# Optimization experiments

Hardware: AMD Instinct MI355X
Metric: run time of the kernel (lower is better)

## Reference

```python
import jax, jax.numpy as jnp
import numpy as np

NU = 160000   # users
NM = 60000    # movies
D = 64        # embedding dim
E = 5000000   # rating edges
L = 200000    # label edges to score
NUM_LAYERS = 3


def setup_inputs() -> dict:
    key = jax.random.key(0)
    k1, k2, k3, k4, k5, k6 = jax.random.split(key, 6)
    return {
        "emb_user": jax.random.normal(k1, (NU, D), jnp.float32),
        "emb_movie": jax.random.normal(k2, (NM, D), jnp.float32),
        "node_id_user": jnp.arange(NU),
        "node_id_movie": jnp.arange(NM),
        "edge_from": jax.random.randint(k3, (E,), 0, NM),   # movie side of each edge
        "edge_to": jax.random.randint(k4, (E,), 0, NU),     # user side of each edge
        "label_movie": jax.random.randint(k5, (L,), 0, NM),
        "label_user": jax.random.randint(k6, (L,), 0, NU),
    }


def reference(emb_user, emb_movie, node_id_user, node_id_movie,
              edge_from, edge_to, label_movie, label_user):
    # Embedding lookup (node_id is an arange over all nodes in the batch)
    x_u = emb_user[node_id_user]    # [NU, D]
    x_m = emb_movie[node_id_movie]  # [NM, D]

    # Symmetric degree normalization: deg(from)^-1/2 * deg(to)^-1/2 per edge
    ones = jnp.ones(edge_from.shape[0], dtype=x_m.dtype)
    deg_m = jax.ops.segment_sum(ones, edge_from, num_segments=NM)
    deg_u = jax.ops.segment_sum(ones, edge_to, num_segments=NU)
    inv_m = jnp.where(deg_m > 0, deg_m ** -0.5, 0.0)
    inv_u = jnp.where(deg_u > 0, deg_u ** -0.5, 0.0)
    norm = inv_m[edge_from] * inv_u[edge_to]  # [E]

    # NOTE: the original torch code never writes the propagated embeddings back
    # into x_dict, so every layer propagates the layer-0 embeddings. Replicated
    # faithfully here.
    embs_u = [x_u]
    embs_m = [x_m]
    for _ in range(NUM_LAYERS):
        # movie -> user aggregation (x2y): gather movie feats, scale, scatter-add to users
        u_agg = jax.ops.segment_sum(norm[:, None] * x_m[edge_from], edge_to, num_segments=NU)
        m_agg = jax.ops.segment_sum(norm[:, None] * x_u[edge_to], edge_from, num_segments=NM)
        embs_u.append(u_agg)
        embs_m.append(m_agg)

    # Layer combination with weights 1/(l+1)
    w = 1.0 / (jnp.arange(NUM_LAYERS + 1, dtype=x_u.dtype) + 1.0)
    res_u = jnp.einsum('l,lnd->nd', w, jnp.stack(embs_u))  # [NU, D]
    res_m = jnp.einsum('l,lnd->nd', w, jnp.stack(embs_m))  # [NM, D]

    # Classifier: dot product over label edges
    scores = jnp.sum(res_u[label_user] * res_m[label_movie], axis=-1)  # [L]
    return (scores, res_u, res_m)
```

## Files before the change

### kernel.cpp

```cpp
#include <hip/hip_runtime.h>

#define NU 160000
#define NM 60000
#define DD 64
#define NE 5000000
#define NL 200000

#define COEF (13.0f / 12.0f)

#define SHIFT_U 9
#define SHIFT_M 7
#define NBU ((NU + (1 << SHIFT_U) - 1) >> SHIFT_U)
#define NBM ((NM + (1 << SHIFT_M) - 1) >> SHIFT_M)


#define CEC 16

__global__ void bucket_count_kernel(const int* __restrict__ ef, const int* __restrict__ et,
                                    int* __restrict__ gbh_u, int* __restrict__ gbh_m) {
    __shared__ int bhu[NBU], bhm[NBM];
    int tid = threadIdx.x;
    for (int i = tid; i < NBU; i += 256) bhu[i] = 0;
    for (int i = tid; i < NBM; i += 256) bhm[i] = 0;
    __syncthreads();
    int base = (blockIdx.x * 256 + tid) * CEC;
    if (base < NE) {
        const int4* f4 = (const int4*)(ef + base);
        const int4* t4 = (const int4*)(et + base);
        #pragma unroll
        for (int q = 0; q < CEC / 4; q++) {
            int4 ff = f4[q]; int4 tt = t4[q];
            atomicAdd(&bhm[ff.x >> SHIFT_M], 1); atomicAdd(&bhu[tt.x >> SHIFT_U], 1);
            atomicAdd(&bhm[ff.y >> SHIFT_M], 1); atomicAdd(&bhu[tt.y >> SHIFT_U], 1);
            atomicAdd(&bhm[ff.z >> SHIFT_M], 1); atomicAdd(&bhu[tt.z >> SHIFT_U], 1);
            atomicAdd(&bhm[ff.w >> SHIFT_M], 1); atomicAdd(&bhu[tt.w >> SHIFT_U], 1);
        }
    }
    __syncthreads();
    for (int i = tid; i < NBU; i += 256) if (bhu[i]) atomicAdd(&gbh_u[i], bhu[i]);
    for (int i = tid; i < NBM; i += 256) if (bhm[i]) atomicAdd(&gbh_m[i], bhm[i]);
}


__global__ void scan_small_kernel(const int* __restrict__ in, int* __restrict__ out,
                                  int* __restrict__ cur, int n) {
    __shared__ int buf[256];
    int tid = threadIdx.x;
    int idx = tid * 4;
    int v0 = (idx + 0 < n) ? in[idx + 0] : 0;
    int v1 = (idx + 1 < n) ? in[idx + 1] : 0;
    int v2 = (idx + 2 < n) ? in[idx + 2] : 0;
    int v3 = (idx + 3 < n) ? in[idx + 3] : 0;
    int s = v0 + v1 + v2 + v3;
    buf[tid] = s;
    __syncthreads();
    for (int off = 1; off < 256; off <<= 1) {
        int t = (tid >= off) ? buf[tid - off] : 0;
        __syncthreads();
        buf[tid] += t;
        __syncthreads();
    }
    int p = buf[tid] - s;
    if (idx + 0 < n) { out[idx + 0] = p; if (cur) cur[idx + 0] = p; p += v0; }
    if (idx + 1 < n) { out[idx + 1] = p; if (cur) cur[idx + 1] = p; p += v1; }
    if (idx + 2 < n) { out[idx + 2] = p; if (cur) cur[idx + 2] = p; p += v2; }
    if (idx + 3 < n) { out[idx + 3] = p; if (cur) cur[idx + 3] = p; p += v3; }
    if (tid == 255) out[n] = buf[255];
}


#define PEC 16

__global__ void partition_kernel(const int* __restrict__ key, const int* __restrict__ val,
                                 int* __restrict__ bcur, int2* __restrict__ stage,
                                 int shift, int nb) {
    __shared__ int lh[512];
    __shared__ int lbase[512];
    int tid = threadIdx.x;
    for (int i = tid; i < nb; i += 256) lh[i] = 0;
    __syncthreads();
    int base = (blockIdx.x * 256 + tid) * PEC;
    int k_[PEC], v_[PEC], br_[PEC];
    bool act = base < NE;
    if (act) {
        const int4* k4 = (const int4*)(key + base);
        const int4* v4 = (const int4*)(val + base);
        #pragma unroll
        for (int q = 0; q < PEC / 4; q++) {
            int4 kk = k4[q]; int4 vv = v4[q];
            k_[q * 4 + 0] = kk.x; k_[q * 4 + 1] = kk.y; k_[q * 4 + 2] = kk.z; k_[q * 4 + 3] = kk.w;
            v_[q * 4 + 0] = vv.x; v_[q * 4 + 1] = vv.y; v_[q * 4 + 2] = vv.z; v_[q * 4 + 3] = vv.w;
        }
        #pragma unroll
        for (int q = 0; q < PEC; q++) {
            int b = k_[q] >> shift;
            int r = atomicAdd(&lh[b], 1);
            br_[q] = (b << 13) | r;
        }
    }
    __syncthreads();
    for (int i = tid; i < nb; i += 256) lbase[i] = lh[i] ? atomicAdd(&bcur[i], lh[i]) : 0;
    __syncthreads();
    if (act) {
        #pragma unroll
        for (int q = 0; q < PEC; q++) {
            int b = br_[q] >> 13;
            int r = br_[q] & 8191;
            stage[lbase[b] + r] = make_int2(k_[q], v_[q]);
        }
    }
}


__global__ void build_kernel(const int2* __restrict__ stage, const int* __restrict__ bo,
                             float* __restrict__ inv, int* __restrict__ rp,
                             int* __restrict__ pay, int shift, int n) {
    __shared__ int cnt[512];
    __shared__ int tmp[512];
    int b = blockIdx.x;
    int tid = threadIdx.x;
    int bs = 1 << shift;
    int base = b << shift;
    int nn = min(bs, n - base);
    int s0 = bo[b];
    int s1 = bo[b + 1];

    for (int i = tid; i < bs; i += 256) cnt[i] = 0;
    __syncthreads();
    for (int e = s0 + tid; e < s1; e += 256)
        atomicAdd(&cnt[stage[e].x - base], 1);
    __syncthreads();
    int o0 = (tid < bs) ? cnt[tid] : 0;
    int o1 = (tid + 256 < bs) ? cnt[tid + 256] : 0;
    for (int off = 1; off < bs; off <<= 1) {
        for (int i = tid; i < bs; i += 256) tmp[i] = (i >= off) ? cnt[i - off] : 0;
        __syncthreads();
        for (int i = tid; i < bs; i += 256) cnt[i] += tmp[i];
        __syncthreads();
    }
    if (tid < bs) {
        int excl = cnt[tid] - o0;
        tmp[tid] = s0 + excl;
        if (tid < nn) {
            rp[base + tid] = s0 + excl;
            inv[base + tid] = (o0 > 0) ? rsqrtf((float)o0) : 0.0f;
        }
    }
    if (tid + 256 < bs) {
        int i = tid + 256;
        int excl = cnt[i] - o1;
        tmp[i] = s0 + excl;
        if (i < nn) {
            rp[base + i] = s0 + excl;
            inv[base + i] = (o1 > 0) ? rsqrtf((float)o1) : 0.0f;
        }
    }
    if (b == 0 && tid == 0) rp[n] = NE;
    __syncthreads();
    for (int e = s0 + tid; e < s1; e += 256) {
        int2 p = stage[e];
        int pos = atomicAdd(&tmp[p.x - base], 1);
        pay[pos] = p.y;
    }
}


__global__ void gather_kernel(const int* __restrict__ rp, const int* __restrict__ pay,
                              const float* __restrict__ inv_dst, const float* __restrict__ inv_src,
                              const float* __restrict__ x_src, const float* __restrict__ x_dst,
                              float* __restrict__ res, int n) {
    int tid = blockIdx.x * blockDim.x + threadIdx.x;
    int node = tid >> 6;
    int lane = threadIdx.x & 63;
    if (node >= n) return;
    int start = rp[node];
    int end   = rp[node + 1];
    float acc = 0.0f;
    for (int i = start; i < end; i += 64) {
        int cnt = min(end - i, 64);
        int nid = (lane < cnt) ? pay[i + lane] : 0;
        int j = 0;
        for (; j + 4 <= cnt; j += 4) {
            int f0 = __shfl(nid, j + 0, 64);
            int f1 = __shfl(nid, j + 1, 64);
            int f2 = __shfl(nid, j + 2, 64);
            int f3 = __shfl(nid, j + 3, 64);
            float w0 = inv_src[f0], w1 = inv_src[f1], w2 = inv_src[f2], w3 = inv_src[f3];
            float a0 = x_src[f0 * DD + lane];
            float a1 = x_src[f1 * DD + lane];
            float a2 = x_src[f2 * DD + lane];
            float a3 = x_src[f3 * DD + lane];
            acc += w0 * a0 + w1 * a1 + w2 * a2 + w3 * a3;
        }
        for (; j < cnt; j++) {
            int f0 = __shfl(nid, j, 64);
            acc += inv_src[f0] * x_src[f0 * DD + lane];
        }
    }
    int o = node * DD + lane;
    res[o] = x_dst[o] + COEF * inv_dst[node] * acc;
}


__global__ void score_kernel(const int* __restrict__ lm, const int* __restrict__ lu,
                             const float* __restrict__ ru, const float* __restrict__ rm,
                             float* __restrict__ scores) {
    int tid = blockIdx.x * blockDim.x + threadIdx.x;
    int l = tid >> 6;
    int d = threadIdx.x & 63;
    if (l < NL) {
        int u = lu[l];
        int m = lm[l];
        float v = ru[u * DD + d] * rm[m * DD + d];
        #pragma unroll
        for (int off = 32; off >= 1; off >>= 1)
            v += __shfl_down(v, off, 64);
        if (d == 0) scores[l] = v;
    }
}


__global__ void degree_kernel_f(const int* __restrict__ ef, const int* __restrict__ et,
                                float* __restrict__ deg_m, float* __restrict__ deg_u) {
    int i = blockIdx.x * blockDim.x + threadIdx.x;
    if (i < NE) {
        atomicAdd(&deg_m[ef[i]], 1.0f);
        atomicAdd(&deg_u[et[i]], 1.0f);
    }
}

__global__ void inv_kernel_f(float* __restrict__ deg, int n) {
    int i = blockIdx.x * blockDim.x + threadIdx.x;
    if (i < n) {
        float d = deg[i];
        deg[i] = (d > 0.0f) ? (1.0f / sqrtf(d)) : 0.0f;
    }
}

__global__ void agg_kernel_f(const int* __restrict__ ef, const int* __restrict__ et,
                             const float* __restrict__ inv_m, const float* __restrict__ inv_u,
                             const float* __restrict__ x_u, const float* __restrict__ x_m,
                             float* __restrict__ res_u, float* __restrict__ res_m) {
    int tid = blockIdx.x * blockDim.x + threadIdx.x;
    int e = tid >> 6;
    int d = tid & 63;
    if (e < NE) {
        int f = ef[e];
        int t = et[e];
        float norm = inv_m[f] * inv_u[t] * COEF;
        atomicAdd(&res_u[t * DD + d], norm * x_m[f * DD + d]);
        atomicAdd(&res_m[f * DD + d], norm * x_u[t * DD + d]);
    }
}

__global__ void add_base_kernel_f(const float* __restrict__ xu, const float* __restrict__ xm,
                                  float* __restrict__ ru, float* __restrict__ rm) {
    int i = blockIdx.x * blockDim.x + threadIdx.x;
    const int nu = NU * DD;
    const int nm = NM * DD;
    if (i < nu) {
        ru[i] += xu[i];
    } else if (i < nu + nm) {
        int j = i - nu;
        rm[j] += xm[j];
    }
}


extern "C" void kernel_launch(void* const* d_in, const int* in_sizes, int n_in,
                              void* d_out, int out_size, void* d_ws, size_t ws_size,
                              hipStream_t stream) {
    const float* emb_user  = (const float*)d_in[0];
    const float* emb_movie = (const float*)d_in[1];
    const int* edge_from   = (const int*)d_in[4];
    const int* edge_to     = (const int*)d_in[5];
    const int* label_movie = (const int*)d_in[6];
    const int* label_user  = (const int*)d_in[7];

    float* out    = (float*)d_out;
    float* scores = out;
    float* res_u  = out + NL;
    float* res_m  = out + NL + (size_t)NU * DD;

    int*   gbh_u  = (int*)d_ws;
    int*   gbh_m  = gbh_u + NBU;
    int*   bo_u   = gbh_m + NBM;
    int*   bcur_u = bo_u + NBU + 1;
    int*   bo_m   = bcur_u + NBU;
    int*   bcur_m = bo_m + NBM + 1;
    float* inv_u  = (float*)(bcur_m + NBM);
    float* inv_m  = inv_u + NU;
    int*   rp_u   = (int*)(inv_m + NM);
    int*   rp_m   = rp_u + NU + 1;
    int*   pay_u  = rp_m + NM + 1;
    int*   pay_m  = pay_u + NE;
    size_t off    = (size_t)((pay_m + NE) - (int*)d_ws);
    off = (off + 3) & ~(size_t)3;
    int2*  stage  = (int2*)((int*)d_ws + off);

    size_t needed = (off + 2 * (size_t)NE) * sizeof(int);

    if (ws_size >= needed) {
        hipMemsetAsync(gbh_u, 0, (size_t)(NBU + NBM) * sizeof(int), stream);

        bucket_count_kernel<<<(NE / CEC + 255) / 256, 256, 0, stream>>>(
            edge_from, edge_to, gbh_u, gbh_m);
        scan_small_kernel<<<1, 256, 0, stream>>>(gbh_u, bo_u, bcur_u, NBU);
        scan_small_kernel<<<1, 256, 0, stream>>>(gbh_m, bo_m, bcur_m, NBM);

        partition_kernel<<<(NE / PEC + 255) / 256, 256, 0, stream>>>(
            edge_to, edge_from, bcur_u, stage, SHIFT_U, NBU);
        build_kernel<<<NBU, 256, 0, stream>>>(stage, bo_u, inv_u, rp_u, pay_u, SHIFT_U, NU);

        partition_kernel<<<(NE / PEC + 255) / 256, 256, 0, stream>>>(
            edge_from, edge_to, bcur_m, stage, SHIFT_M, NBM);
        build_kernel<<<NBM, 256, 0, stream>>>(stage, bo_m, inv_m, rp_m, pay_m, SHIFT_M, NM);

        gather_kernel<<<((size_t)NU * 64 + 255) / 256, 256, 0, stream>>>(
            rp_u, pay_u, inv_u, inv_m, emb_movie, emb_user, res_u, NU);
        gather_kernel<<<((size_t)NM * 64 + 255) / 256, 256, 0, stream>>>(
            rp_m, pay_m, inv_m, inv_u, emb_user, emb_movie, res_m, NM);
    } else {
        float* fdeg_u = (float*)d_ws;
        float* fdeg_m = fdeg_u + NU;
        hipMemsetAsync(res_u, 0, (size_t)(NU + NM) * DD * sizeof(float), stream);
        hipMemsetAsync(fdeg_u, 0, (size_t)(NU + NM) * sizeof(float), stream);
        degree_kernel_f<<<(NE + 255) / 256, 256, 0, stream>>>(edge_from, edge_to, fdeg_m, fdeg_u);
        inv_kernel_f<<<(NU + NM + 255) / 256, 256, 0, stream>>>(fdeg_u, NU + NM);
        agg_kernel_f<<<((size_t)NE * 64 + 255) / 256, 256, 0, stream>>>(
            edge_from, edge_to, fdeg_m, fdeg_u, emb_user, emb_movie, res_u, res_m);
        add_base_kernel_f<<<((NU + NM) * DD + 255) / 256, 256, 0, stream>>>(
            emb_user, emb_movie, res_u, res_m);
    }

    score_kernel<<<((size_t)NL * 64 + 255) / 256, 256, 0, stream>>>(
        label_movie, label_user, res_u, res_m, scores);
}
```

Measured before the change: 749.5 us.

## Pack staging edges into one int and gather bf16 pre-scaled source features

Edge staging now packs the local destination index and the source id into a single 32-bit word instead of an int2, which halves staging traffic in partition and build. A new prescale kernel multiplies each source embedding by its inverse-sqrt degree and stores the result as bf16. The gather then reads half-width rows with no per-edge weight lookup. This cuts the random-gather bandwidth, at the cost of bf16 rounding error in the aggregated embeddings and an extra prescale pass that reuses the staging buffer region.

```diff
diff --git a/kernel.cpp b/kernel.cpp
--- a/kernel.cpp
+++ b/kernel.cpp
@@ -1,4 +1,5 @@
 #include <hip/hip_runtime.h>
+#include <hip/hip_bf16.h>
 
 #define NU 160000
 #define NM 60000
@@ -12,6 +13,8 @@
 #define SHIFT_M 7
 #define NBU ((NU + (1 << SHIFT_U) - 1) >> SHIFT_U)
 #define NBM ((NM + (1 << SHIFT_M) - 1) >> SHIFT_M)
+#define VB_U 16
+#define VB_M 18
 
 
 #define CEC 16
@@ -72,11 +75,12 @@
 #define PEC 16
 
 __global__ void partition_kernel(const int* __restrict__ key, const int* __restrict__ val,
-                                 int* __restrict__ bcur, int2* __restrict__ stage,
-                                 int shift, int nb) {
+                                 int* __restrict__ bcur, int* __restrict__ stage,
+                                 int shift, int nb, int valbits) {
     __shared__ int lh[512];
     __shared__ int lbase[512];
     int tid = threadIdx.x;
+    int lmask = (1 << shift) - 1;
     for (int i = tid; i < nb; i += 256) lh[i] = 0;
     __syncthreads();
     int base = (blockIdx.x * 256 + tid) * PEC;
@@ -106,15 +110,15 @@
         for (int q = 0; q < PEC; q++) {
             int b = br_[q] >> 13;
             int r = br_[q] & 8191;
-            stage[lbase[b] + r] = make_int2(k_[q], v_[q]);
-        }
-    }
-}
-
-
-__global__ void build_kernel(const int2* __restrict__ stage, const int* __restrict__ bo,
+            stage[lbase[b] + r] = ((k_[q] & lmask) << valbits) | v_[q];
+        }
+    }
+}
+
+
+__global__ void build_kernel(const int* __restrict__ stage, const int* __restrict__ bo,
                              float* __restrict__ inv, int* __restrict__ rp,
-                             int* __restrict__ pay, int shift, int n) {
+                             int* __restrict__ pay, int shift, int n, int valbits) {
     __shared__ int cnt[512];
     __shared__ int tmp[512];
     int b = blockIdx.x;
@@ -122,13 +126,14 @@
     int bs = 1 << shift;
     int base = b << shift;
     int nn = min(bs, n - base);
+    int vmask = (1 << valbits) - 1;
     int s0 = bo[b];
     int s1 = bo[b + 1];
 
     for (int i = tid; i < bs; i += 256) cnt[i] = 0;
     __syncthreads();
     for (int e = s0 + tid; e < s1; e += 256)
-        atomicAdd(&cnt[stage[e].x - base], 1);
+        atomicAdd(&cnt[stage[e] >> valbits], 1);
     __syncthreads();
     int o0 = (tid < bs) ? cnt[tid] : 0;
     int o1 = (tid + 256 < bs) ? cnt[tid + 256] : 0;
@@ -158,16 +163,27 @@
     if (b == 0 && tid == 0) rp[n] = NE;
     __syncthreads();
     for (int e = s0 + tid; e < s1; e += 256) {
-        int2 p = stage[e];
-        int pos = atomicAdd(&tmp[p.x - base], 1);
-        pay[pos] = p.y;
+        int p = stage[e];
+        int pos = atomicAdd(&tmp[p >> valbits], 1);
+        pay[pos] = p & vmask;
+    }
+}
+
+
+__global__ void prescale_kernel(const float* __restrict__ x, const float* __restrict__ inv,
+                                __hip_bfloat16* __restrict__ y, int total) {
+    int i = blockIdx.x * blockDim.x + threadIdx.x;
+    if (i < total) {
+        int node = i >> 6;
+        y[i] = __float2bfloat16(inv[node] * x[i]);
     }
 }
 
 
 __global__ void gather_kernel(const int* __restrict__ rp, const int* __restrict__ pay,
-                              const float* __restrict__ inv_dst, const float* __restrict__ inv_src,
-                              const float* __restrict__ x_src, const float* __restrict__ x_dst,
+                              const float* __restrict__ inv_dst,
+                              const __hip_bfloat16* __restrict__ y_src,
+                              const float* __restrict__ x_dst,
                               float* __restrict__ res, int n) {
     int tid = blockIdx.x * blockDim.x + threadIdx.x;
     int node = tid >> 6;
@@ -185,16 +201,15 @@
             int f1 = __shfl(nid, j + 1, 64);
             int f2 = __shfl(nid, j + 2, 64);
             int f3 = __shfl(nid, j + 3, 64);
-            float w0 = inv_src[f0], w1 = inv_src[f1], w2 = inv_src[f2], w3 = inv_src[f3];
-            float a0 = x_src[f0 * DD + lane];
-            float a1 = x_src[f1 * DD + lane];
-            float a2 = x_src[f2 * DD + lane];
-            float a3 = x_src[f3 * DD + lane];
-            acc += w0 * a0 + w1 * a1 + w2 * a2 + w3 * a3;
+            float a0 = __bfloat162float(y_src[f0 * DD + lane]);
+            float a1 = __bfloat162float(y_src[f1 * DD + lane]);
+            float a2 = __bfloat162float(y_src[f2 * DD + lane]);
+            float a3 = __bfloat162float(y_src[f3 * DD + lane]);
+            acc += a0 + a1 + a2 + a3;
         }
         for (; j < cnt; j++) {
             int f0 = __shfl(nid, j, 64);
-            acc += inv_src[f0] * x_src[f0 * DD + lane];
+            acc += __bfloat162float(y_src[f0 * DD + lane]);
         }
     }
     int o = node * DD + lane;
@@ -294,11 +309,14 @@
     int*   rp_m   = rp_u + NU + 1;
     int*   pay_u  = rp_m + NM + 1;
     int*   pay_m  = pay_u + NE;
-    size_t off    = (size_t)((pay_m + NE) - (int*)d_ws);
-    off = (off + 3) & ~(size_t)3;
-    int2*  stage  = (int2*)((int*)d_ws + off);
-
-    size_t needed = (off + 2 * (size_t)NE) * sizeof(int);
+    int*   ureg   = pay_m + NE;
+    int*   stage  = ureg;
+    __hip_bfloat16* y_u = (__hip_bfloat16*)ureg;
+    __hip_bfloat16* y_m = (__hip_bfloat16*)(ureg + (size_t)NU * DD / 2);
+
+    size_t ysz    = (size_t)(NU + NM) * DD / 2;
+    size_t uni    = (size_t)NE > ysz ? (size_t)NE : ysz;
+    size_t needed = ((size_t)(ureg - (int*)d_ws) + uni) * sizeof(int);
 
     if (ws_size >= needed) {
         hipMemsetAsync(gbh_u, 0, (size_t)(NBU + NBM) * sizeof(int), stream);
@@ -309,17 +327,22 @@
         scan_small_kernel<<<1, 256, 0, stream>>>(gbh_m, bo_m, bcur_m, NBM);
 
         partition_kernel<<<(NE / PEC + 255) / 256, 256, 0, stream>>>(
-            edge_to, edge_from, bcur_u, stage, SHIFT_U, NBU);
-        build_kernel<<<NBU, 256, 0, stream>>>(stage, bo_u, inv_u, rp_u, pay_u, SHIFT_U, NU);
+            edge_to, edge_from, bcur_u, stage, SHIFT_U, NBU, VB_U);
+        build_kernel<<<NBU, 256, 0, stream>>>(stage, bo_u, inv_u, rp_u, pay_u, SHIFT_U, NU, VB_U);
 
         partition_kernel<<<(NE / PEC + 255) / 256, 256, 0, stream>>>(
-            edge_from, edge_to, bcur_m, stage, SHIFT_M, NBM);
-        build_kernel<<<NBM, 256, 0, stream>>>(stage, bo_m, inv_m, rp_m, pay_m, SHIFT_M, NM);
+            edge_from, edge_to, bcur_m, stage, SHIFT_M, NBM, VB_M);
+        build_kernel<<<NBM, 256, 0, stream>>>(stage, bo_m, inv_m, rp_m, pay_m, SHIFT_M, NM, VB_M);
+
+        prescale_kernel<<<((size_t)NU * DD + 255) / 256, 256, 0, stream>>>(
+            emb_user, inv_u, y_u, NU * DD);
+        prescale_kernel<<<((size_t)NM * DD + 255) / 256, 256, 0, stream>>>(
+            emb_movie, inv_m, y_m, NM * DD);
 
         gather_kernel<<<((size_t)NU * 64 + 255) / 256, 256, 0, stream>>>(
-            rp_u, pay_u, inv_u, inv_m, emb_movie, emb_user, res_u, NU);
+            rp_u, pay_u, inv_u, y_m, emb_user, res_u, NU);
         gather_kernel<<<((size_t)NM * 64 + 255) / 256, 256, 0, stream>>>(
-            rp_m, pay_m, inv_m, inv_u, emb_user, emb_movie, res_m, NM);
+            rp_m, pay_m, inv_m, y_u, emb_movie, res_m, NM);
     } else {
         float* fdeg_u = (float*)d_ws;
         float* fdeg_m = fdeg_u + NU;
```

After: 717.2 us. 4.3% less time.
